# Kernel tuning notes

Hardware: AMD Instinct MI355X
Metric: run time of the kernel (lower is better)

## Reference

```python
import jax, jax.numpy as jnp
import numpy as np

T, B, I, H = 2048, 256, 64, 128


def setup_inputs() -> dict:
    key = jax.random.key(0)
    ks = jax.random.split(key, 12)
    s_i = 1.0 / np.sqrt(I)
    s_h = 1.0 / np.sqrt(H)
    return {
        "x": jax.random.normal(ks[0], (T, B, I), dtype=jnp.float32),
        # input->hidden kernels (with bias), flax GRUCell naming ir/iz/in
        "Wir": jax.random.normal(ks[1], (I, H), dtype=jnp.float32) * s_i,
        "Wiz": jax.random.normal(ks[2], (I, H), dtype=jnp.float32) * s_i,
        "Win": jax.random.normal(ks[3], (I, H), dtype=jnp.float32) * s_i,
        "bir": jnp.zeros((H,), dtype=jnp.float32),
        "biz": jnp.zeros((H,), dtype=jnp.float32),
        "bin": jnp.zeros((H,), dtype=jnp.float32),
        # hidden->hidden kernels: hr/hz no bias, hn has bias (flax GRUCell)
        "Whr": jax.random.normal(ks[4], (H, H), dtype=jnp.float32) * s_h,
        "Whz": jax.random.normal(ks[5], (H, H), dtype=jnp.float32) * s_h,
        "Whn": jax.random.normal(ks[6], (H, H), dtype=jnp.float32) * s_h,
        "bhn": jnp.zeros((H,), dtype=jnp.float32),
        # classifier Linear(H, 1)
        "Wc": jax.random.normal(ks[7], (H, 1), dtype=jnp.float32) * s_h,
        "bc": jnp.zeros((1,), dtype=jnp.float32),
    }


def reference(x, Wir, Wiz, Win, bir, biz, bin, Whr, Whz, Whn, bhn, Wc, bc):
    # GRU scan over time (time-major), flax GRUCell math:
    # r = sig(x Wir + bir + h Whr); z = sig(x Wiz + biz + h Whz)
    def step(h, xt):
        r = jax.nn.sigmoid(xt @ Wir + bir + h @ Whr)
        z = jax.nn.sigmoid(xt @ Wiz + biz + h @ Whz)
        n = jnp.tanh(xt @ Win + bin + r * (h @ Whn + bhn))
        h_new = (1.0 - z) * n + z * h
        return h_new, h_new

    h0 = jnp.zeros((x.shape[1], Whr.shape[0]), dtype=x.dtype)
    _, hs = jax.lax.scan(step, h0, x)  # hs: [T, B, H]
    return jax.nn.sigmoid(hs @ Wc + bc)  # [T, B, 1]
```

## Files before the change

kernel.cpp:

```cpp
#include <hip/hip_runtime.h>

#define TT 2048
#define BB 256
#define II 64
#define HH 128
#define CHP 16
#define NCH (TT / CHP)
#define GXS 532

#define LOG2E  1.4426950408889634f
#define LOG2E2 2.8853900817779268f

typedef __fp16 f16;
typedef __fp16 h2  __attribute__((ext_vector_type(2)));
typedef __fp16 v8h __attribute__((ext_vector_type(8)));
typedef float  v4f __attribute__((ext_vector_type(4)));

union HI { int i; h2 h; };
__device__ __forceinline__ h2  i2h(int v) { HI u; u.i = v; return u.h; }
__device__ __forceinline__ int h2i(h2 v)  { HI u; u.h = v; return u.i; }

__device__ __forceinline__ float fexp2(float x) {
  float r; asm("v_exp_f32 %0, %1" : "=v"(r) : "v"(x)); return r;
}
__device__ __forceinline__ float fsig(float x) {
  return __builtin_amdgcn_rcpf(1.0f + __expf(-x));
}

__device__ __forceinline__ void bar_lgkm() {
  asm volatile("s_waitcnt lgkmcnt(0)\n\ts_barrier" ::: "memory");
}

template <int CLS>
__global__ __launch_bounds__(512, 1) void gru_mfma(
    const float* __restrict__ x,
    const float* __restrict__ Wir, const float* __restrict__ Wiz, const float* __restrict__ Win,
    const float* __restrict__ bir, const float* __restrict__ biz, const float* __restrict__ bin_,
    const float* __restrict__ Whr, const float* __restrict__ Whz, const float* __restrict__ Whn,
    const float* __restrict__ bhn, const float* __restrict__ Wc,  const float* __restrict__ bc,
    f16* __restrict__ hh, float* __restrict__ out)
{
  const int t = threadIdx.x, b = blockIdx.x;
  const int w = t >> 6;
  const int l = t & 63;
  const int q = l >> 4;
  const int r = l & 15;
  const int nc = 16 * w + r;

  __shared__ __attribute__((aligned(16))) f16   hbuf[2][HH];
  __shared__ __attribute__((aligned(16))) f16   xch[2][CHP][72];
  __shared__ __attribute__((aligned(16))) float gxb[2][CHP][GXS];
  __shared__ float cpart[2][128];

  v8h br_[6], bz_[6], bnh_[4], bnx_[2];
  for (int kt = 0; kt < 6; ++kt) {
    v8h vr, vz;
    for (int j = 0; j < 8; ++j) {
      const int kg = 32 * kt + 8 * q + j;
      vr[j] = (f16)(LOG2E * ((kg < HH) ? Whr[kg * HH + nc] : Wir[(kg - HH) * HH + nc]));
      vz[j] = (f16)(LOG2E * ((kg < HH) ? Whz[kg * HH + nc] : Wiz[(kg - HH) * HH + nc]));
    }
    br_[kt] = vr; bz_[kt] = vz;
  }
  for (int kt = 0; kt < 4; ++kt) {
    v8h v;
    for (int j = 0; j < 8; ++j) v[j] = (f16)(LOG2E2 * Whn[(32 * kt + 8 * q + j) * HH + nc]);
    bnh_[kt] = v;
  }
  for (int kt = 0; kt < 2; ++kt) {
    v8h v;
    for (int j = 0; j < 8; ++j) v[j] = (f16)(LOG2E2 * Win[(32 * kt + 8 * q + j) * HH + nc]);
    bnx_[kt] = v;
  }

  const float birc = LOG2E * bir[nc],  bizc = LOG2E * biz[nc];
  const float binc = LOG2E2 * bin_[nc], bhnc = LOG2E2 * bhn[nc];
  float wc = 0.f, bc0 = 0.f;
  if (CLS == 1) { wc = Wc[nc]; bc0 = bc[0]; }

  auto precomp_full = [&](int pn, v8h ax0, v8h ax1) {
    v4f cr = {birc, birc, birc, birc};
    v4f cz = {bizc, bizc, bizc, bizc};
    v4f cn = {binc, binc, binc, binc};
    cr = __builtin_amdgcn_mfma_f32_16x16x32_f16(ax0, br_[4],  cr, 0, 0, 0);
    cz = __builtin_amdgcn_mfma_f32_16x16x32_f16(ax0, bz_[4],  cz, 0, 0, 0);
    cn = __builtin_amdgcn_mfma_f32_16x16x32_f16(ax0, bnx_[0], cn, 0, 0, 0);
    cr = __builtin_amdgcn_mfma_f32_16x16x32_f16(ax1, br_[5],  cr, 0, 0, 0);
    cz = __builtin_amdgcn_mfma_f32_16x16x32_f16(ax1, bz_[5],  cz, 0, 0, 0);
    cn = __builtin_amdgcn_mfma_f32_16x16x32_f16(ax1, bnx_[1], cn, 0, 0, 0);
    #pragma unroll
    for (int j = 0; j < 4; ++j) {
      v4f pk; pk[0] = cr[j]; pk[1] = cz[j]; pk[2] = cn[j]; pk[3] = 0.f;
      *(v4f*)&gxb[pn][4 * q + j][nc * 4] = pk;
    }
  };

  const int xrow = t >> 5, xcol = (t & 31) * 2;
  float2 xr;
  {
    float2 xA = *(const float2*)(x + ((size_t)(0   + xrow) * BB + b) * II + xcol);
    float2 xB = *(const float2*)(x + ((size_t)(CHP + xrow) * BB + b) * II + xcol);
    if (t < HH) { hbuf[0][t] = (f16)0.f; hbuf[1][t] = (f16)0.f; }
    *(int*)&xch[0][xrow][xcol] = h2i(__builtin_amdgcn_cvt_pkrtz(xA.x, xA.y));
    __syncthreads();
    {
      v8h a0x = *(const v8h*)&xch[0][r][8 * q];
      v8h a1x = *(const v8h*)&xch[0][r][32 + 8 * q];
      precomp_full(0, a0x, a1x);
    }
    *(int*)&xch[1][xrow][xcol] = h2i(__builtin_amdgcn_cvt_pkrtz(xB.x, xB.y));
    __syncthreads();
  }

  v4f gp = *(const v4f*)&gxb[0][0][nc * 4];

  v8h af[4] = {};
  float hst = 0.f;
  f16* hup = (CLS == 0) ? (hh + (size_t)b * HH) : nullptr;
  v4f cpr, cpz, cpn;

  for (int c = 0; c < NCH; ++c) {
    const int p = c & 1;
    const bool pc = (c + 1 < NCH);
    const bool ld = (c + 2 < NCH);

    v8h ax0 = {}, ax1 = {};
    if (pc) {
      ax0 = *(const v8h*)&xch[p ^ 1][r][8 * q];
      ax1 = *(const v8h*)&xch[p ^ 1][r][32 + 8 * q];
    }
    if (ld) {
      xr = *(const float2*)(x + ((size_t)((c + 2) * CHP + xrow) * BB + b) * II + xcol);
    }

    #pragma unroll
    for (int sc = 0; sc < CHP; ++sc) {
      const int s = c * CHP + sc;
      const int cur = sc & 1, nxt = cur ^ 1;

      if (r == 0) {
        af[0] = *(const v8h*)&hbuf[cur][8 * q];
        af[1] = *(const v8h*)&hbuf[cur][32 + 8 * q];
        af[2] = *(const v8h*)&hbuf[cur][64 + 8 * q];
        af[3] = *(const v8h*)&hbuf[cur][96 + 8 * q];
      }

      if (pc) {
        if (sc == 0) {
          v4f ir = {birc, birc, birc, birc};
          cpr = __builtin_amdgcn_mfma_f32_16x16x32_f16(ax0, br_[4], ir, 0, 0, 0);
        } else if (sc == 1) {
          v4f iz = {bizc, bizc, bizc, bizc};
          cpz = __builtin_amdgcn_mfma_f32_16x16x32_f16(ax0, bz_[4], iz, 0, 0, 0);
        } else if (sc == 2) {
          v4f in_ = {binc, binc, binc, binc};
          cpn = __builtin_amdgcn_mfma_f32_16x16x32_f16(ax0, bnx_[0], in_, 0, 0, 0);
        } else if (sc == 3) {
          cpr = __builtin_amdgcn_mfma_f32_16x16x32_f16(ax1, br_[5], cpr, 0, 0, 0);
        } else if (sc == 4) {
          cpz = __builtin_amdgcn_mfma_f32_16x16x32_f16(ax1, bz_[5], cpz, 0, 0, 0);
        } else if (sc == 5) {
          cpn = __builtin_amdgcn_mfma_f32_16x16x32_f16(ax1, bnx_[1], cpn, 0, 0, 0);
        } else if (sc >= 6 && sc < 10) {
          const int j = sc - 6;
          v4f pk; pk[0] = cpr[j]; pk[1] = cpz[j]; pk[2] = cpn[j]; pk[3] = 0.f;
          *(v4f*)&gxb[p ^ 1][4 * q + j][nc * 4] = pk;
        }
      }

      float cred = 0.f;
      if (CLS == 1 && w == 7 && (sc > 0 || c > 0))
        cred = cpart[nxt][l] + cpart[nxt][64 + l];

      const v4f vz0 = {0.f, 0.f, 0.f, 0.f};
      v4f ar0, ar1, an0, an1, az0, az1;
      ar0 = __builtin_amdgcn_mfma_f32_16x16x32_f16(af[0], br_[0],  vz0, 0, 0, 0);
      an0 = __builtin_amdgcn_mfma_f32_16x16x32_f16(af[0], bnh_[0], vz0, 0, 0, 0);
      ar0 = __builtin_amdgcn_mfma_f32_16x16x32_f16(af[1], br_[1],  ar0, 0, 0, 0);
      an0 = __builtin_amdgcn_mfma_f32_16x16x32_f16(af[1], bnh_[1], an0, 0, 0, 0);
      ar1 = __builtin_amdgcn_mfma_f32_16x16x32_f16(af[2], br_[2],  vz0, 0, 0, 0);
      an1 = __builtin_amdgcn_mfma_f32_16x16x32_f16(af[2], bnh_[2], vz0, 0, 0, 0);
      ar1 = __builtin_amdgcn_mfma_f32_16x16x32_f16(af[3], br_[3],  ar1, 0, 0, 0);
      an1 = __builtin_amdgcn_mfma_f32_16x16x32_f16(af[3], bnh_[3], an1, 0, 0, 0);
      az0 = __builtin_amdgcn_mfma_f32_16x16x32_f16(af[0], bz_[0],  vz0, 0, 0, 0);
      az1 = __builtin_amdgcn_mfma_f32_16x16x32_f16(af[2], bz_[2],  vz0, 0, 0, 0);
      az0 = __builtin_amdgcn_mfma_f32_16x16x32_f16(af[1], bz_[1],  az0, 0, 0, 0);
      az1 = __builtin_amdgcn_mfma_f32_16x16x32_f16(af[3], bz_[3],  az1, 0, 0, 0);

      const v4f g = gp;
      if (sc < CHP - 1) {
        gp = *(const v4f*)&gxb[p][sc + 1][nc * 4];
      } else if (c + 1 < NCH) {
        gp = *(const v4f*)&gxb[p ^ 1][0][nc * 4];
      }

      if (q == 0) {
        const float arS = ar0[0] + ar1[0] + g[0];
        const float rr  = __builtin_amdgcn_rcpf(1.f + fexp2(-arS));
        const float anS = an0[0] + an1[0] + bhnc;
        const float nn  = 1.f - 2.f * __builtin_amdgcn_rcpf(1.f + fexp2(g[2] + rr * anS));
        const float azS = az0[0] + az1[0] + g[1];
        const float zz  = __builtin_amdgcn_rcpf(1.f + fexp2(-azS));
        hst = nn + zz * (hst - nn);
        const f16 hf = (f16)hst;
        hbuf[nxt][nc] = hf;
        if (CLS == 0) hup[nc] = hf;
        if (CLS == 1) cpart[cur][nc] = hst * wc;
      }
      if (CLS == 0) hup += BB * HH;

      if (CLS == 1 && w == 7 && (sc > 0 || c > 0)) {
        cred += __shfl_xor(cred, 1, 64);
        cred += __shfl_xor(cred, 2, 64);
        cred += __shfl_xor(cred, 4, 64);
        cred += __shfl_xor(cred, 8, 64);
        cred += __shfl_xor(cred, 16, 64);
        cred += __shfl_xor(cred, 32, 64);
        if (l == 0) out[(size_t)(s - 1) * BB + b] = fsig(cred + bc0);
      }

      if (sc == CHP - 1 && ld) {
        *(int*)&xch[p][xrow][xcol] = h2i(__builtin_amdgcn_cvt_pkrtz(xr.x, xr.y));
      }

      bar_lgkm();
    }
  }

  if (CLS == 1 && w == 7) {
    float cred = cpart[1][l] + cpart[1][64 + l];
    cred += __shfl_xor(cred, 1, 64);
    cred += __shfl_xor(cred, 2, 64);
    cred += __shfl_xor(cred, 4, 64);
    cred += __shfl_xor(cred, 8, 64);
    cred += __shfl_xor(cred, 16, 64);
    cred += __shfl_xor(cred, 32, 64);
    if (l == 0) out[(size_t)(TT - 1) * BB + b] = fsig(cred + bc0);
  }
}

__global__ __launch_bounds__(256) void gru_cls(
    const f16* __restrict__ hh, const float* __restrict__ Wc,
    const float* __restrict__ bc, float* __restrict__ out)
{
  const int t  = threadIdx.x;
  const int g4 = t & 3;
  const size_t row = (size_t)blockIdx.x * 64 + (t >> 2);
  const f16* hp = hh + row * HH + 32 * g4;
  const float* wp = Wc + 32 * g4;
  float acc = 0.f;
  #pragma unroll
  for (int i = 0; i < 4; ++i) {
    v8h h8 = *(const v8h*)(hp + 8 * i);
    const float* wq = wp + 8 * i;
    #pragma unroll
    for (int j = 0; j < 8; ++j) acc += (float)h8[j] * wq[j];
  }
  acc += __shfl_xor(acc, 1, 64);
  acc += __shfl_xor(acc, 2, 64);
  if (g4 == 0) out[row] = fsig(acc + bc[0]);
}

extern "C" void kernel_launch(void* const* d_in, const int* in_sizes, int n_in,
                              void* d_out, int out_size, void* d_ws, size_t ws_size,
                              hipStream_t stream) {
  const float* x    = (const float*)d_in[0];
  const float* Wir  = (const float*)d_in[1];
  const float* Wiz  = (const float*)d_in[2];
  const float* Win  = (const float*)d_in[3];
  const float* bir  = (const float*)d_in[4];
  const float* biz  = (const float*)d_in[5];
  const float* bin_ = (const float*)d_in[6];
  const float* Whr  = (const float*)d_in[7];
  const float* Whz  = (const float*)d_in[8];
  const float* Whn  = (const float*)d_in[9];
  const float* bhn  = (const float*)d_in[10];
  const float* Wc   = (const float*)d_in[11];
  const float* bc   = (const float*)d_in[12];
  float* out = (float*)d_out;

  const size_t need = (size_t)TT * BB * HH * sizeof(f16);
  if (d_ws != nullptr && ws_size >= need) {
    f16* hh = (f16*)d_ws;
    gru_mfma<0><<<dim3(BB), dim3(512), 0, stream>>>(
        x, Wir, Wiz, Win, bir, biz, bin_, Whr, Whz, Whn, bhn, Wc, bc, hh, out);
    gru_cls<<<dim3((TT * BB) / 64), dim3(256), 0, stream>>>(hh, Wc, bc, out);
  } else {
    gru_mfma<1><<<dim3(BB), dim3(512), 0, stream>>>(
        x, Wir, Wiz, Win, bir, biz, bin_, Whr, Whz, Whn, bhn, Wc, bc, nullptr, out);
  }
}
```

Before: 866.6 us.

## Quantize recurrent hidden-state matmul to int8 MFMA with per-column weight scales

Replaces the f16 hidden-to-hidden MFMA chain with int8 16x16x64 MFMAs. The recurrent weights are quantized per output column using an absmax scale, and the hidden state is stored in shared memory as int8 scaled by 127. This halves the number of MFMAs on the serial per-step critical path and shrinks the hidden-state LDS reads. In exchange it adds significant quantization error to the recurrence, which may accumulate over 2048 steps and break accuracy tolerance.

```diff
diff --git a/kernel.cpp b/kernel.cpp
--- a/kernel.cpp
+++ b/kernel.cpp
@@ -15,6 +15,7 @@
 typedef __fp16 h2  __attribute__((ext_vector_type(2)));
 typedef __fp16 v8h __attribute__((ext_vector_type(8)));
 typedef float  v4f __attribute__((ext_vector_type(4)));
+typedef int    v4i __attribute__((ext_vector_type(4)));
 
 union HI { int i; h2 h; };
 __device__ __forceinline__ h2  i2h(int v) { HI u; u.i = v; return u.h; }
@@ -47,30 +48,51 @@
   const int r = l & 15;
   const int nc = 16 * w + r;
 
-  __shared__ __attribute__((aligned(16))) f16   hbuf[2][HH];
+  __shared__ __attribute__((aligned(16))) signed char hq8[2][HH];
   __shared__ __attribute__((aligned(16))) f16   xch[2][CHP][72];
   __shared__ __attribute__((aligned(16))) float gxb[2][CHP][GXS];
   __shared__ float cpart[2][128];
 
-  v8h br_[6], bz_[6], bnh_[4], bnx_[2];
-  for (int kt = 0; kt < 6; ++kt) {
-    v8h vr, vz;
+  v4i bqr[2], bqz[2], bqn[2];
+  float invR, invZ, invN;
+  {
+    float mr = 1e-20f, mz = 1e-20f, mn = 1e-20f;
+    for (int f = 0; f < 2; ++f)
+      for (int j = 0; j < 16; ++j) {
+        const int k = 64 * f + 16 * q + j;
+        mr = fmaxf(mr, fabsf(Whr[k * HH + nc]));
+        mz = fmaxf(mz, fabsf(Whz[k * HH + nc]));
+        mn = fmaxf(mn, fabsf(Whn[k * HH + nc]));
+      }
+    mr = fmaxf(mr, __shfl_xor(mr, 16, 64)); mr = fmaxf(mr, __shfl_xor(mr, 32, 64));
+    mz = fmaxf(mz, __shfl_xor(mz, 16, 64)); mz = fmaxf(mz, __shfl_xor(mz, 32, 64));
+    mn = fmaxf(mn, __shfl_xor(mn, 16, 64)); mn = fmaxf(mn, __shfl_xor(mn, 32, 64));
+    const float sr = 127.f / mr, sz = 127.f / mz, sn = 127.f / mn;
+    invR = LOG2E  * mr / 16129.f;
+    invZ = LOG2E  * mz / 16129.f;
+    invN = LOG2E2 * mn / 16129.f;
+    for (int f = 0; f < 2; ++f) {
+      union { signed char c[16]; v4i v; } ur, uz, un;
+      for (int j = 0; j < 16; ++j) {
+        const int k = 64 * f + 16 * q + j;
+        ur.c[j] = (signed char)(int)rintf(Whr[k * HH + nc] * sr);
+        uz.c[j] = (signed char)(int)rintf(Whz[k * HH + nc] * sz);
+        un.c[j] = (signed char)(int)rintf(Whn[k * HH + nc] * sn);
+      }
+      bqr[f] = ur.v; bqz[f] = uz.v; bqn[f] = un.v;
+    }
+  }
+
+  v8h wir[2], wiz[2], win2[2];
+  for (int kt = 0; kt < 2; ++kt) {
+    v8h vr, vz, vn;
     for (int j = 0; j < 8; ++j) {
       const int kg = 32 * kt + 8 * q + j;
-      vr[j] = (f16)(LOG2E * ((kg < HH) ? Whr[kg * HH + nc] : Wir[(kg - HH) * HH + nc]));
-      vz[j] = (f16)(LOG2E * ((kg < HH) ? Whz[kg * HH + nc] : Wiz[(kg - HH) * HH + nc]));
-    }
-    br_[kt] = vr; bz_[kt] = vz;
-  }
-  for (int kt = 0; kt < 4; ++kt) {
-    v8h v;
-    for (int j = 0; j < 8; ++j) v[j] = (f16)(LOG2E2 * Whn[(32 * kt + 8 * q + j) * HH + nc]);
-    bnh_[kt] = v;
-  }
-  for (int kt = 0; kt < 2; ++kt) {
-    v8h v;
-    for (int j = 0; j < 8; ++j) v[j] = (f16)(LOG2E2 * Win[(32 * kt + 8 * q + j) * HH + nc]);
-    bnx_[kt] = v;
+      vr[j] = (f16)(LOG2E  * Wir[kg * HH + nc]);
+      vz[j] = (f16)(LOG2E  * Wiz[kg * HH + nc]);
+      vn[j] = (f16)(LOG2E2 * Win[kg * HH + nc]);
+    }
+    wir[kt] = vr; wiz[kt] = vz; win2[kt] = vn;
   }
 
   const float birc = LOG2E * bir[nc],  bizc = LOG2E * biz[nc];
@@ -82,12 +104,12 @@
     v4f cr = {birc, birc, birc, birc};
     v4f cz = {bizc, bizc, bizc, bizc};
     v4f cn = {binc, binc, binc, binc};
-    cr = __builtin_amdgcn_mfma_f32_16x16x32_f16(ax0, br_[4],  cr, 0, 0, 0);
-    cz = __builtin_amdgcn_mfma_f32_16x16x32_f16(ax0, bz_[4],  cz, 0, 0, 0);
-    cn = __builtin_amdgcn_mfma_f32_16x16x32_f16(ax0, bnx_[0], cn, 0, 0, 0);
-    cr = __builtin_amdgcn_mfma_f32_16x16x32_f16(ax1, br_[5],  cr, 0, 0, 0);
-    cz = __builtin_amdgcn_mfma_f32_16x16x32_f16(ax1, bz_[5],  cz, 0, 0, 0);
-    cn = __builtin_amdgcn_mfma_f32_16x16x32_f16(ax1, bnx_[1], cn, 0, 0, 0);
+    cr = __builtin_amdgcn_mfma_f32_16x16x32_f16(ax0, wir[0],  cr, 0, 0, 0);
+    cz = __builtin_amdgcn_mfma_f32_16x16x32_f16(ax0, wiz[0],  cz, 0, 0, 0);
+    cn = __builtin_amdgcn_mfma_f32_16x16x32_f16(ax0, win2[0], cn, 0, 0, 0);
+    cr = __builtin_amdgcn_mfma_f32_16x16x32_f16(ax1, wir[1],  cr, 0, 0, 0);
+    cz = __builtin_amdgcn_mfma_f32_16x16x32_f16(ax1, wiz[1],  cz, 0, 0, 0);
+    cn = __builtin_amdgcn_mfma_f32_16x16x32_f16(ax1, win2[1], cn, 0, 0, 0);
     #pragma unroll
     for (int j = 0; j < 4; ++j) {
       v4f pk; pk[0] = cr[j]; pk[1] = cz[j]; pk[2] = cn[j]; pk[3] = 0.f;
@@ -100,7 +122,7 @@
   {
     float2 xA = *(const float2*)(x + ((size_t)(0   + xrow) * BB + b) * II + xcol);
     float2 xB = *(const float2*)(x + ((size_t)(CHP + xrow) * BB + b) * II + xcol);
-    if (t < HH) { hbuf[0][t] = (f16)0.f; hbuf[1][t] = (f16)0.f; }
+    if (t < HH) { hq8[0][t] = 0; hq8[1][t] = 0; }
     *(int*)&xch[0][xrow][xcol] = h2i(__builtin_amdgcn_cvt_pkrtz(xA.x, xA.y));
     __syncthreads();
     {
@@ -114,7 +136,7 @@
 
   v4f gp = *(const v4f*)&gxb[0][0][nc * 4];
 
-  v8h af[4] = {};
+  v4i ai0 = {0, 0, 0, 0}, ai1 = {0, 0, 0, 0};
   float hst = 0.f;
   f16* hup = (CLS == 0) ? (hh + (size_t)b * HH) : nullptr;
   v4f cpr, cpz, cpn;
@@ -139,28 +161,26 @@
       const int cur = sc & 1, nxt = cur ^ 1;
 
       if (r == 0) {
-        af[0] = *(const v8h*)&hbuf[cur][8 * q];
-        af[1] = *(const v8h*)&hbuf[cur][32 + 8 * q];
-        af[2] = *(const v8h*)&hbuf[cur][64 + 8 * q];
-        af[3] = *(const v8h*)&hbuf[cur][96 + 8 * q];
+        ai0 = *(const v4i*)&hq8[cur][16 * q];
+        ai1 = *(const v4i*)&hq8[cur][64 + 16 * q];
       }
 
       if (pc) {
         if (sc == 0) {
           v4f ir = {birc, birc, birc, birc};
-          cpr = __builtin_amdgcn_mfma_f32_16x16x32_f16(ax0, br_[4], ir, 0, 0, 0);
+          cpr = __builtin_amdgcn_mfma_f32_16x16x32_f16(ax0, wir[0], ir, 0, 0, 0);
         } else if (sc == 1) {
           v4f iz = {bizc, bizc, bizc, bizc};
-          cpz = __builtin_amdgcn_mfma_f32_16x16x32_f16(ax0, bz_[4], iz, 0, 0, 0);
+          cpz = __builtin_amdgcn_mfma_f32_16x16x32_f16(ax0, wiz[0], iz, 0, 0, 0);
         } else if (sc == 2) {
           v4f in_ = {binc, binc, binc, binc};
-          cpn = __builtin_amdgcn_mfma_f32_16x16x32_f16(ax0, bnx_[0], in_, 0, 0, 0);
+          cpn = __builtin_amdgcn_mfma_f32_16x16x32_f16(ax0, win2[0], in_, 0, 0, 0);
         } else if (sc == 3) {
-          cpr = __builtin_amdgcn_mfma_f32_16x16x32_f16(ax1, br_[5], cpr, 0, 0, 0);
+          cpr = __builtin_amdgcn_mfma_f32_16x16x32_f16(ax1, wir[1], cpr, 0, 0, 0);
         } else if (sc == 4) {
-          cpz = __builtin_amdgcn_mfma_f32_16x16x32_f16(ax1, bz_[5], cpz, 0, 0, 0);
+          cpz = __builtin_amdgcn_mfma_f32_16x16x32_f16(ax1, wiz[1], cpz, 0, 0, 0);
         } else if (sc == 5) {
-          cpn = __builtin_amdgcn_mfma_f32_16x16x32_f16(ax1, bnx_[1], cpn, 0, 0, 0);
+          cpn = __builtin_amdgcn_mfma_f32_16x16x32_f16(ax1, win2[1], cpn, 0, 0, 0);
         } else if (sc >= 6 && sc < 10) {
           const int j = sc - 6;
           v4f pk; pk[0] = cpr[j]; pk[1] = cpz[j]; pk[2] = cpn[j]; pk[3] = 0.f;
@@ -172,20 +192,14 @@
       if (CLS == 1 && w == 7 && (sc > 0 || c > 0))
         cred = cpart[nxt][l] + cpart[nxt][64 + l];
 
-      const v4f vz0 = {0.f, 0.f, 0.f, 0.f};
-      v4f ar0, ar1, an0, an1, az0, az1;
-      ar0 = __builtin_amdgcn_mfma_f32_16x16x32_f16(af[0], br_[0],  vz0, 0, 0, 0);
-      an0 = __builtin_amdgcn_mfma_f32_16x16x32_f16(af[0], bnh_[0], vz0, 0, 0, 0);
-      ar0 = __builtin_amdgcn_mfma_f32_16x16x32_f16(af[1], br_[1],  ar0, 0, 0, 0);
-      an0 = __builtin_amdgcn_mfma_f32_16x16x32_f16(af[1], bnh_[1], an0, 0, 0, 0);
-      ar1 = __builtin_amdgcn_mfma_f32_16x16x32_f16(af[2], br_[2],  vz0, 0, 0, 0);
-      an1 = __builtin_amdgcn_mfma_f32_16x16x32_f16(af[2], bnh_[2], vz0, 0, 0, 0);
-      ar1 = __builtin_amdgcn_mfma_f32_16x16x32_f16(af[3], br_[3],  ar1, 0, 0, 0);
-      an1 = __builtin_amdgcn_mfma_f32_16x16x32_f16(af[3], bnh_[3], an1, 0, 0, 0);
-      az0 = __builtin_amdgcn_mfma_f32_16x16x32_f16(af[0], bz_[0],  vz0, 0, 0, 0);
-      az1 = __builtin_amdgcn_mfma_f32_16x16x32_f16(af[2], bz_[2],  vz0, 0, 0, 0);
-      az0 = __builtin_amdgcn_mfma_f32_16x16x32_f16(af[1], bz_[1],  az0, 0, 0, 0);
-      az1 = __builtin_amdgcn_mfma_f32_16x16x32_f16(af[3], bz_[3],  az1, 0, 0, 0);
+      const v4i zi = {0, 0, 0, 0};
+      v4i cr_, cn2, cz_;
+      cr_ = __builtin_amdgcn_mfma_i32_16x16x64_i8(ai0, bqr[0], zi, 0, 0, 0);
+      cn2 = __builtin_amdgcn_mfma_i32_16x16x64_i8(ai0, bqn[0], zi, 0, 0, 0);
+      cz_ = __builtin_amdgcn_mfma_i32_16x16x64_i8(ai0, bqz[0], zi, 0, 0, 0);
+      cr_ = __builtin_amdgcn_mfma_i32_16x16x64_i8(ai1, bqr[1], cr_, 0, 0, 0);
+      cn2 = __builtin_amdgcn_mfma_i32_16x16x64_i8(ai1, bqn[1], cn2, 0, 0, 0);
+      cz_ = __builtin_amdgcn_mfma_i32_16x16x64_i8(ai1, bqz[1], cz_, 0, 0, 0);
 
       const v4f g = gp;
       if (sc < CHP - 1) {
@@ -195,16 +209,15 @@
       }
 
       if (q == 0) {
-        const float arS = ar0[0] + ar1[0] + g[0];
+        const float arS = (float)cr_[0] * invR + g[0];
         const float rr  = __builtin_amdgcn_rcpf(1.f + fexp2(-arS));
-        const float anS = an0[0] + an1[0] + bhnc;
+        const float anS = (float)cn2[0] * invN + bhnc;
         const float nn  = 1.f - 2.f * __builtin_amdgcn_rcpf(1.f + fexp2(g[2] + rr * anS));
-        const float azS = az0[0] + az1[0] + g[1];
+        const float azS = (float)cz_[0] * invZ + g[1];
         const float zz  = __builtin_amdgcn_rcpf(1.f + fexp2(-azS));
         hst = nn + zz * (hst - nn);
-        const f16 hf = (f16)hst;
-        hbuf[nxt][nc] = hf;
-        if (CLS == 0) hup[nc] = hf;
+        hq8[nxt][nc] = (signed char)(int)rintf(hst * 127.f);
+        if (CLS == 0) hup[nc] = (f16)hst;
         if (CLS == 1) cpart[cur][nc] = hst * wc;
       }
       if (CLS == 0) hup += BB * HH;
```

Measured after the change: 768.5 us, median of 2. 11.3% less time.
